# Kernel tuning notes

Hardware: AMD Instinct MI355X
Metric: run time of the kernel (lower is better)

The kernel has to match this reference:

```python
import jax, jax.numpy as jnp
import numpy as np

B, S, C = 32, 1024, 12      # sentences, words per sentence, chars per word
E, H = 256, 512             # embedding dim, word-LSTM hidden dim
V, CS, T = 50000, 128, 50   # vocab, charset, tagset


def _lstm(x, Wih, Whh, b):
    """Standard torch LSTM (gate order i,f,g,o). x: [T, N, I] -> hidden trace [T, N, H]."""
    Hd = Whh.shape[1]
    N = x.shape[1]
    h0 = jnp.zeros((N, Hd), x.dtype)
    c0 = jnp.zeros((N, Hd), x.dtype)

    def step(carry, xt):
        h, c = carry
        gates = xt @ Wih.T + h @ Whh.T + b
        i, f, g, o = jnp.split(gates, 4, axis=-1)
        c = jax.nn.sigmoid(f) * c + jax.nn.sigmoid(i) * jnp.tanh(g)
        h = jax.nn.sigmoid(o) * jnp.tanh(c)
        return (h, c), h

    _, hs = jax.lax.scan(step, (h0, c0), x)
    return hs


def setup_inputs() -> dict:
    key = jax.random.key(0)
    ks = jax.random.split(key, 12)
    sc = 0.05
    return {
        "char_idx": jax.random.randint(ks[0], (B, S, C), 0, CS),
        "word_idx": jax.random.randint(ks[1], (B, S), 0, V),
        "char_emb": jax.random.normal(ks[2], (CS, E), jnp.float32) * sc,
        "word_emb": jax.random.normal(ks[3], (V, E), jnp.float32) * sc,
        "Wc_ih": jax.random.normal(ks[4], (4 * E, E), jnp.float32) * sc,
        "Wc_hh": jax.random.normal(ks[5], (4 * E, E), jnp.float32) * sc,
        "bc": jnp.zeros((4 * E,), jnp.float32),
        "Ww_ih": jax.random.normal(ks[6], (4 * H, 2 * E), jnp.float32) * sc,
        "Ww_hh": jax.random.normal(ks[7], (4 * H, H), jnp.float32) * sc,
        "bw": jnp.zeros((4 * H,), jnp.float32),
        "Wt": jax.random.normal(ks[8], (T, H), jnp.float32) * sc,
        "bt": jnp.zeros((T,), jnp.float32),
    }


def reference(char_idx, word_idx, char_emb, word_emb, Wc_ih, Wc_hh, bc,
              Ww_ih, Ww_hh, bw, Wt, bt):
    # --- character-level LSTM: each word starts from a fresh zero state ---
    ce = char_emb[char_idx]                       # [B, S, C, E]
    ce = ce.reshape(B * S, C, E).transpose(1, 0, 2)  # [C, B*S, E]
    char_hs = _lstm(ce, Wc_ih, Wc_hh, bc)         # [C, B*S, E]
    char_feat = char_hs[-1].reshape(B, S, E)      # last char output per word

    # --- word-level LSTM over concatenated [word_emb ; char_feat] ---
    we = word_emb[word_idx]                       # [B, S, E]
    x = jnp.concatenate([we, char_feat], axis=-1) # [B, S, 2E]
    x = x.transpose(1, 0, 2)                      # [S, B, 2E]
    word_hs = _lstm(x, Ww_ih, Ww_hh, bw)          # [S, B, H]
    word_hs = word_hs.transpose(1, 0, 2)          # [B, S, H]

    # --- tag projection + log_softmax per token ---
    logits = word_hs @ Wt.T + bt                  # [B, S, T]
    return jax.nn.log_softmax(logits, axis=-1)
```

## Files before the change

### kernel.cpp

```cpp
#include <hip/hip_runtime.h>
#include <stdint.h>
#include <stddef.h>

#define NB   32
#define NS   1024
#define NC   12
#define NE   256
#define NH   512
#define NT   50
#define NWRD 32768
#define MC   1024
#define RW   2048
#define KW   512

typedef short bf16x8 __attribute__((ext_vector_type(8)));
typedef short bf16x4 __attribute__((ext_vector_type(4)));
typedef float f32x4  __attribute__((ext_vector_type(4)));
typedef unsigned int u32x4 __attribute__((ext_vector_type(4)));

#define MFMA16(a,b,c) __builtin_amdgcn_mfma_f32_16x16x32_bf16(a, b, c, 0, 0, 0)

__device__ __forceinline__ float bf2f(short u){
  return __uint_as_float(((uint32_t)(uint16_t)u) << 16);
}
__device__ __forceinline__ short f2bf(float f){
  uint32_t u = __float_as_uint(f);
  uint32_t r = (u + 0x7FFFu + ((u >> 16) & 1u)) >> 16;
  return (short)r;
}
__device__ __forceinline__ float sigf(float x){
  float e = __expf(-fabsf(x));
  float s = 1.0f / (1.0f + e);
  return x >= 0.0f ? s : 1.0f - s;
}
__device__ __forceinline__ float tanh_f(float x){
  float e = __expf(-2.0f * fabsf(x));
  float r = (1.0f - e) / (1.0f + e);
  return x >= 0.0f ? r : -r;
}
__device__ __forceinline__ uint32_t agent_ld(const uint32_t* p){
  return __hip_atomic_load(p, __ATOMIC_RELAXED, __HIP_MEMORY_SCOPE_AGENT);
}
__device__ __forceinline__ void agent_st(uint32_t* p, uint32_t v){
  __hip_atomic_store(p, v, __ATOMIC_RELAXED, __HIP_MEMORY_SCOPE_AGENT);
}

__global__ __launch_bounds__(256) void k_prep_pe(
    const float* __restrict__ char_emb, const float* __restrict__ Wc_ih,
    const float* __restrict__ bc, float* __restrict__ PEb)
{
  __shared__ float ce[NE];
  int a = blockIdx.x, tid = threadIdx.x;
  ce[tid] = char_emb[a * NE + tid];
  __syncthreads();
  int j = tid;
  float acc[4];
  #pragma unroll
  for (int g = 0; g < 4; ++g) acc[g] = 0.0f;
  for (int k = 0; k < NE; ++k) {
    float c = ce[k];
    #pragma unroll
    for (int g = 0; g < 4; ++g)
      acc[g] += c * Wc_ih[(size_t)(g * NE + j) * NE + k];
  }
  float4 o;
  o.x = acc[0] + bc[0 * NE + j];
  o.y = acc[1] + bc[1 * NE + j];
  o.z = acc[2] + bc[2 * NE + j];
  o.w = acc[3] + bc[3 * NE + j];
  *(float4*)&PEb[(size_t)a * MC + j * 4] = o;
}

__global__ __launch_bounds__(256) void k_prep_w(
    const float* __restrict__ Wc_hh, const float* __restrict__ Ww_ih,
    const float* __restrict__ Ww_hh, const float* __restrict__ bw,
    short* __restrict__ WhhC, short* __restrict__ WihW,
    short* __restrict__ WhhW, float* __restrict__ bwI)
{
  int r = blockIdx.x;
  int j = r >> 2, g = r & 3, tid = threadIdx.x;
  if (r < MC) {
    float v = Wc_hh[(size_t)(g * NE + j) * NE + tid];
    WhhC[(size_t)r * NE + tid] = f2bf(v);
  }
  #pragma unroll
  for (int kk = 0; kk < 2; ++kk) {
    int k = tid + kk * 256;
    WihW[(size_t)r * KW + k] = f2bf(Ww_ih[(size_t)(g * NH + j) * KW + k]);
    WhhW[(size_t)r * NH + k] = f2bf(Ww_hh[(size_t)(g * NH + j) * NH + k]);
  }
  if (tid == 0) bwI[r] = bw[g * NH + j];
}

__global__ __launch_bounds__(256) void k_char0(
    const int* __restrict__ char_idx, const float* __restrict__ PEb,
    float* __restrict__ c_state, short* __restrict__ h_out)
{
  int w = blockIdx.x, j = threadIdx.x;
  int idx = char_idx[w * NC + 0];
  float4 pe = *(const float4*)&PEb[(size_t)idx * MC + j * 4];
  float c = sigf(pe.x) * tanh_f(pe.z);
  float h = sigf(pe.w) * tanh_f(c);
  c_state[(size_t)w * NE + j] = c;
  h_out[(size_t)w * NE + j] = f2bf(h);
}

template<int KDIM, int EPI>
__global__ __launch_bounds__(256) void gemm_epi(
    const short* __restrict__ Amat, const short* __restrict__ Bmat,
    const float* __restrict__ PEb, const int* __restrict__ char_idx, int tstep,
    float* __restrict__ c_state, short* __restrict__ h_out,
    const float* __restrict__ bias, short* __restrict__ pw_out)
{
  __shared__ __align__(16) short As[128 * 64];
  __shared__ __align__(16) short Bs[128 * 64];
  const int tid = threadIdx.x;
  const int lane = tid & 63;
  const int wid = tid >> 6;
  const int wm = wid >> 1, wn = wid & 1;
  const int m0 = blockIdx.y * 128;
  const int n0 = blockIdx.x * 128;
  const int lo = lane & 15, hi = lane >> 4;

  f32x4 acc[4][4];
  #pragma unroll
  for (int i = 0; i < 4; ++i)
    #pragma unroll
    for (int j = 0; j < 4; ++j) acc[i][j] = (f32x4)0.0f;

  const int nk = KDIM / 64;
  for (int ki = 0; ki < nk; ++ki) {
    __syncthreads();
    #pragma unroll
    for (int it = 0; it < 4; ++it) {
      int cid = tid + it * 256;
      int row = cid >> 3, cp = cid & 7;
      int kch = cp ^ (row & 7);
      *(bf16x8*)&As[row * 64 + cp * 8] =
          *(const bf16x8*)&Amat[(size_t)(m0 + row) * KDIM + ki * 64 + kch * 8];
      *(bf16x8*)&Bs[row * 64 + cp * 8] =
          *(const bf16x8*)&Bmat[(size_t)(n0 + row) * KDIM + ki * 64 + kch * 8];
    }
    __syncthreads();
    #pragma unroll
    for (int kc = 0; kc < 2; ++kc) {
      bf16x8 af[4], bfr[4];
      #pragma unroll
      for (int fm = 0; fm < 4; ++fm) {
        int row = wm * 64 + fm * 16 + lo;
        int ch = (kc * 4 + hi) ^ (row & 7);
        af[fm] = *(bf16x8*)&As[row * 64 + ch * 8];
      }
      #pragma unroll
      for (int fn = 0; fn < 4; ++fn) {
        int row = wn * 64 + fn * 16 + lo;
        int ch = (kc * 4 + hi) ^ (row & 7);
        bfr[fn] = *(bf16x8*)&Bs[row * 64 + ch * 8];
      }
      #pragma unroll
      for (int fm = 0; fm < 4; ++fm)
        #pragma unroll
        for (int fn = 0; fn < 4; ++fn)
          acc[fm][fn] = MFMA16(af[fm], bfr[fn], acc[fm][fn]);
    }
  }

  #pragma unroll
  for (int fm = 0; fm < 4; ++fm) {
    int r0 = m0 + wm * 64 + fm * 16 + hi * 4;
    #pragma unroll
    for (int fn = 0; fn < 4; ++fn) {
      int w = n0 + wn * 64 + fn * 16 + lo;
      if constexpr (EPI == 0) {
        int idx = char_idx[w * NC + tstep];
        float4 pe = *(const float4*)&PEb[(size_t)idx * MC + r0];
        float gi = acc[fm][fn][0] + pe.x;
        float gf = acc[fm][fn][1] + pe.y;
        float gg = acc[fm][fn][2] + pe.z;
        float go = acc[fm][fn][3] + pe.w;
        int j = r0 >> 2;
        float c = sigf(gf) * c_state[(size_t)w * NE + j] + sigf(gi) * tanh_f(gg);
        c_state[(size_t)w * NE + j] = c;
        h_out[(size_t)w * NE + j] = f2bf(sigf(go) * tanh_f(c));
      } else {
        float4 bb = *(const float4*)&bias[r0];
        bf16x4 o;
        o[0] = f2bf(acc[fm][fn][0] + bb.x);
        o[1] = f2bf(acc[fm][fn][1] + bb.y);
        o[2] = f2bf(acc[fm][fn][2] + bb.z);
        o[3] = f2bf(acc[fm][fn][3] + bb.w);
        *(bf16x4*)&pw_out[(size_t)w * RW + r0] = o;
      }
    }
  }
}

__global__ __launch_bounds__(64) void k_xw(
    const int* __restrict__ word_idx, const float* __restrict__ word_emb,
    const short* __restrict__ h_char, short* __restrict__ Xw)
{
  int wp = blockIdx.x;
  int s = wp >> 5, b = wp & 31;
  int w = b * NS + s;
  int tid = threadIdx.x;
  int widx = word_idx[w];
  #pragma unroll
  for (int g = 0; g < 2; ++g) {
    int k4 = (tid + g * 64) * 4;
    bf16x4 o;
    if (k4 < NE) {
      float4 v = *(const float4*)&word_emb[(size_t)widx * NE + k4];
      o[0] = f2bf(v.x); o[1] = f2bf(v.y); o[2] = f2bf(v.z); o[3] = f2bf(v.w);
    } else {
      o = *(const bf16x4*)&h_char[(size_t)w * NE + (k4 - NE)];
    }
    *(bf16x4*)&Xw[(size_t)wp * KW + k4] = o;
  }
}

template<bool FAST>
__device__ __forceinline__ void word_loop(
    const short* __restrict__ Whh, const short* __restrict__ PW,
    short* hdat, uint32_t* flags, short* __restrict__ word_hs,
    short* h_lds, int bk, int tid)
{
  const int lane = tid & 63, wv = tid >> 6;
  const int lo = lane & 15, hi = lane >> 4;
  const int wr = wv >> 1, wc = wv & 1;
  const int rowbase = bk * 64 + wr * 16;
  const int b = wc * 16 + lo;
  const int jl = (rowbase >> 2) + hi;
  const int r4 = rowbase + hi * 4;

  bf16x8 a[16];
  #pragma unroll
  for (int kc = 0; kc < 16; ++kc)
    a[kc] = *(const bf16x8*)&Whh[(size_t)(rowbase + lo) * NH + kc * 32 + hi * 8];

  const int db = tid >> 4, dlo = (tid & 15) * 8;
  const short* dA = hdat + db * 512 + dlo;
  const short* dB = dA + 16384;
  const uint32_t* fA = flags + (lane & 31);
  const uint32_t* fB = fA + 64;

  float cst = 0.0f;
  bf16x4 pw  = *(const bf16x4*)&PW[(size_t)(0 * NB + b) * RW + r4];
  bf16x4 pw1 = *(const bf16x4*)&PW[(size_t)(1 * NB + b) * RW + r4];

  for (int s = 0; s < NS; ++s) {
    const uint32_t tv = (uint32_t)s;
    const int par = s & 1;

    {
      const uint32_t* fp = par ? fB : fA;
      int tries = 0;
      for (;;) {
        uint32_t f;
        if constexpr (FAST)
          asm volatile("global_load_dword %0, %1, off sc0\n\t"
                       "s_waitcnt vmcnt(0)" : "=&v"(f) : "v"(fp));
        else
          asm volatile("global_load_dword %0, %1, off sc1\n\t"
                       "s_waitcnt vmcnt(0)" : "=&v"(f) : "v"(fp));
        if (__ballot(f == tv) == ~0ull) break;
        if constexpr (!FAST) {
          if (++tries > 768) {
            if (__ballot(agent_ld(fp) == tv) == ~0ull) break;
            tries = 0;
          }
        }
        __builtin_amdgcn_s_sleep(1);
      }
    }

    const short* sp = par ? dB : dA;
    bf16x8 d0, d1, d2, d3;
    if constexpr (FAST)
      asm volatile("global_load_dwordx4 %0, %4, off sc0\n\t"
                   "global_load_dwordx4 %1, %4, off offset:256 sc0\n\t"
                   "global_load_dwordx4 %2, %4, off offset:512 sc0\n\t"
                   "global_load_dwordx4 %3, %4, off offset:768 sc0\n\t"
                   "s_waitcnt vmcnt(0)"
                   : "=&v"(d0), "=&v"(d1), "=&v"(d2), "=&v"(d3) : "v"(sp));
    else
      asm volatile("global_load_dwordx4 %0, %4, off sc1\n\t"
                   "global_load_dwordx4 %1, %4, off offset:256 sc1\n\t"
                   "global_load_dwordx4 %2, %4, off offset:512 sc1\n\t"
                   "global_load_dwordx4 %3, %4, off offset:768 sc1\n\t"
                   "s_waitcnt vmcnt(0)"
                   : "=&v"(d0), "=&v"(d1), "=&v"(d2), "=&v"(d3) : "v"(sp));

    int s2 = (s + 2 < NS) ? (s + 2) : (NS - 1);
    bf16x4 pw2 = *(const bf16x4*)&PW[(size_t)(s2 * NB + b) * RW + r4];

    short* buf = h_lds + par * (32 * 520);
    short* dst = buf + db * 520 + dlo;
    *(bf16x8*)&dst[0]   = d0;
    *(bf16x8*)&dst[128] = d1;
    *(bf16x8*)&dst[256] = d2;
    *(bf16x8*)&dst[384] = d3;
    __syncthreads();

    f32x4 acc0, acc1, acc2, acc3;
    #pragma unroll
    for (int q = 0; q < 4; ++q) {
      acc0[q] = bf2f(pw[q]); acc1[q] = 0.0f; acc2[q] = 0.0f; acc3[q] = 0.0f;
    }
    #pragma unroll
    for (int kc = 0; kc < 16; kc += 4) {
      bf16x8 h0 = *(bf16x8*)((const char*)buf + b * 1040 + (kc + 0) * 64 + hi * 16);
      bf16x8 h1 = *(bf16x8*)((const char*)buf + b * 1040 + (kc + 1) * 64 + hi * 16);
      bf16x8 h2 = *(bf16x8*)((const char*)buf + b * 1040 + (kc + 2) * 64 + hi * 16);
      bf16x8 h3 = *(bf16x8*)((const char*)buf + b * 1040 + (kc + 3) * 64 + hi * 16);
      acc0 = MFMA16(a[kc + 0], h0, acc0);
      acc1 = MFMA16(a[kc + 1], h1, acc1);
      acc2 = MFMA16(a[kc + 2], h2, acc2);
      acc3 = MFMA16(a[kc + 3], h3, acc3);
    }
    f32x4 acc;
    #pragma unroll
    for (int q = 0; q < 4; ++q) acc[q] = (acc0[q] + acc1[q]) + (acc2[q] + acc3[q]);

    float c = sigf(acc[1]) * cst + sigf(acc[0]) * tanh_f(acc[2]);
    cst = c;
    short hv = f2bf(sigf(acc[3]) * tanh_f(c));

    unsigned int own = (unsigned int)(unsigned short)hv;
    unsigned int part = (unsigned int)__shfl_xor((int)own, 16);
    const int npar = (s + 1) & 1;
    if ((hi & 1) == 0) {
      unsigned int val = own | (part << 16);
      short* hp = hdat + (npar << 14) + b * 512 + jl;
      if constexpr (FAST)
        asm volatile("global_store_dword %0, %1, off sc0" :: "v"(hp), "v"(val) : "memory");
      else
        asm volatile("global_store_dword %0, %1, off sc1" :: "v"(hp), "v"(val) : "memory");
    }
    asm volatile("s_waitcnt vmcnt(0)" ::: "memory");
    __syncthreads();
    if (tid == 0) {
      uint32_t* fq = flags + npar * 64 + bk;
      if constexpr (FAST)
        asm volatile("global_store_dword %0, %1, off sc0"
                     :: "v"(fq), "v"((uint32_t)(s + 1)) : "memory");
      else
        asm volatile("global_store_dword %0, %1, off sc1"
                     :: "v"(fq), "v"((uint32_t)(s + 1)) : "memory");
    }
    word_hs[((size_t)b * NS + s) * NH + jl] = hv;
    pw = pw1; pw1 = pw2;
  }
}

__global__ __launch_bounds__(512, 2) void k_word(
    const short* __restrict__ Whh,
    const short* __restrict__ PW,
    uint8_t* __restrict__ xb,
    short* __restrict__ word_hs)
{
  __shared__ __align__(16) short h_lds[2 * 32 * 520];
  __shared__ int sh_bk, sh_fast;
  const int tid = threadIdx.x;

  short*    hdat  = (short*)xb;
  uint32_t* flags = (uint32_t*)(xb + 65536);
  uint32_t* cnt   = (uint32_t*)(xb + 66048);
  uint32_t* win   = (uint32_t*)(xb + 66080);
  uint32_t* probe = (uint32_t*)(xb + 66112);
  uint32_t* rdy1  = (uint32_t*)(xb + 66240);
  uint32_t* ack1  = (uint32_t*)(xb + 66368);
  uint32_t* rdy2  = (uint32_t*)(xb + 66496);
  uint32_t* verd  = (uint32_t*)(xb + 66624);

  if (tid == 0) {
    uint32_t xcc;
    asm volatile("s_getreg_b32 %0, hwreg(HW_REG_XCC_ID)" : "=s"(xcc));
    xcc &= 7u;
    uint32_t slot = __hip_atomic_fetch_add(&cnt[xcc], 1u, __ATOMIC_RELAXED,
                                           __HIP_MEMORY_SCOPE_AGENT);
    if (slot == 31u) {
      uint32_t exp = 0u;
      __hip_atomic_compare_exchange_strong(win, &exp, xcc + 1u, __ATOMIC_RELAXED,
                                           __ATOMIC_RELAXED, __HIP_MEMORY_SCOPE_AGENT);
    }
    uint32_t w;
    for (;;) {
      w = agent_ld(win);
      if (w != 0u) break;
      __builtin_amdgcn_s_sleep(8);
    }
    sh_bk = (w == xcc + 1u && slot < 32u) ? (int)slot : -1;
  }
  __syncthreads();
  const int bk = sh_bk;
  if (bk < 0) return;

  if (tid == 0) {
    if (bk == 0) {
      asm volatile("global_store_dword %0, %1, off sc0" :: "v"(probe), "v"(0x11111111u) : "memory");
      asm volatile("s_waitcnt vmcnt(0)" ::: "memory");
      agent_st(rdy1, 1u);
      uint32_t a;
      for (;;) { a = agent_ld(ack1); if (a != 0u) break; __builtin_amdgcn_s_sleep(4); }
      if (a == 1u) {
        asm volatile("global_store_dword %0, %1, off sc0" :: "v"(probe), "v"(0x22222222u) : "memory");
        asm volatile("s_waitcnt vmcnt(0)" ::: "memory");
        agent_st(rdy2, 1u);
      }
    } else if (bk == 31) {
      for (;;) { if (agent_ld(rdy1) != 0u) break; __builtin_amdgcn_s_sleep(4); }
      bool okA = false;
      for (int i = 0; i < 192 && !okA; ++i) {
        uint32_t pv;
        asm volatile("global_load_dword %0, %1, off sc0\n\ts_waitcnt vmcnt(0)"
                     : "=&v"(pv) : "v"(probe));
        okA = (pv == 0x11111111u);
        if (!okA) __builtin_amdgcn_s_sleep(2);
      }
      agent_st(ack1, okA ? 1u : 2u);
      bool okB = false;
      if (okA) {
        for (;;) { if (agent_ld(rdy2) != 0u) break; __builtin_amdgcn_s_sleep(4); }
        for (int i = 0; i < 192 && !okB; ++i) {
          uint32_t pv;
          asm volatile("global_load_dword %0, %1, off sc0\n\ts_waitcnt vmcnt(0)"
                       : "=&v"(pv) : "v"(probe));
          okB = (pv == 0x22222222u);
          if (!okB) __builtin_amdgcn_s_sleep(2);
        }
      }
      agent_st(verd, okB ? 1u : 2u);
    }
    uint32_t v;
    for (;;) { v = agent_ld(verd); if (v != 0u) break; __builtin_amdgcn_s_sleep(4); }
    sh_fast = (v == 1u);
  }
  __syncthreads();

  if (sh_fast)
    word_loop<true >(Whh, PW, hdat, flags, word_hs, h_lds, bk, tid);
  else
    word_loop<false>(Whh, PW, hdat, flags, word_hs, h_lds, bk, tid);
}

__global__ __launch_bounds__(256) void k_tags(
    const short* __restrict__ word_hs, const float* __restrict__ Wt,
    const float* __restrict__ bt, float* __restrict__ out)
{
  __shared__ __align__(16) short Ws[64 * 256];
  const int tid = threadIdx.x, lane = tid & 63, wid = tid >> 6;
  const int lo = lane & 15, hi = lane >> 4;
  const int n0 = blockIdx.x * 128;
  const int wb = n0 + wid * 32;

  f32x4 acc[4][2];
  #pragma unroll
  for (int fm = 0; fm < 4; ++fm)
    #pragma unroll
    for (int fn = 0; fn < 2; ++fn) acc[fm][fn] = (f32x4)0.0f;

  for (int half = 0; half < 2; ++half) {
    __syncthreads();
    for (int cid = tid; cid < 2048; cid += 256) {
      int row = cid >> 5, cp = cid & 31;
      int kch = cp ^ (row & 7);
      bf16x8 v;
      if (row < NT) {
        const float* src = &Wt[(size_t)row * KW + half * 256 + kch * 8];
        #pragma unroll
        for (int e = 0; e < 8; ++e) v[e] = f2bf(src[e]);
      } else v = (bf16x8)0;
      *(bf16x8*)&Ws[row * 256 + cp * 8] = v;
    }
    __syncthreads();
    #pragma unroll
    for (int kc = 0; kc < 8; ++kc) {
      bf16x8 bfr[2];
      #pragma unroll
      for (int fn = 0; fn < 2; ++fn) {
        int w = wb + fn * 16 + lo;
        bfr[fn] = *(const bf16x8*)&word_hs[(size_t)w * KW + half * 256 + kc * 32 + hi * 8];
      }
      #pragma unroll
      for (int fm = 0; fm < 4; ++fm) {
        int row = fm * 16 + lo;
        int ch = (kc * 4 + hi) ^ (row & 7);
        bf16x8 av = *(bf16x8*)&Ws[row * 256 + ch * 8];
        acc[fm][0] = MFMA16(av, bfr[0], acc[fm][0]);
        acc[fm][1] = MFMA16(av, bfr[1], acc[fm][1]);
      }
    }
  }

  #pragma unroll
  for (int fn = 0; fn < 2; ++fn) {
    int w = wb + fn * 16 + lo;
    float lg[16];
    float m = -1e30f;
    #pragma unroll
    for (int fm = 0; fm < 4; ++fm)
      #pragma unroll
      for (int q = 0; q < 4; ++q) {
        int tg = fm * 16 + hi * 4 + q;
        float bv = (tg < NT) ? bt[tg] : 0.0f;
        float v = acc[fm][fn][q] + bv;
        lg[fm * 4 + q] = v;
        if (tg < NT) m = fmaxf(m, v);
      }
    m = fmaxf(m, __shfl_xor(m, 16));
    m = fmaxf(m, __shfl_xor(m, 32));
    float s = 0.0f;
    #pragma unroll
    for (int fm = 0; fm < 4; ++fm)
      #pragma unroll
      for (int q = 0; q < 4; ++q) {
        int tg = fm * 16 + hi * 4 + q;
        if (tg < NT) s += __expf(lg[fm * 4 + q] - m);
      }
    s += __shfl_xor(s, 16);
    s += __shfl_xor(s, 32);
    float lz = m + __logf(s);
    #pragma unroll
    for (int fm = 0; fm < 4; ++fm)
      #pragma unroll
      for (int q = 0; q < 4; ++q) {
        int tg = fm * 16 + hi * 4 + q;
        if (tg < NT) out[(size_t)w * NT + tg] = lg[fm * 4 + q] - lz;
      }
  }
}

extern "C" void kernel_launch(void* const* d_in, const int* in_sizes, int n_in,
                              void* d_out, int out_size, void* d_ws, size_t ws_size,
                              hipStream_t stream) {
  const int*   char_idx = (const int*)  d_in[0];
  const int*   word_idx = (const int*)  d_in[1];
  const float* char_emb = (const float*)d_in[2];
  const float* word_emb = (const float*)d_in[3];
  const float* Wc_ih    = (const float*)d_in[4];
  const float* Wc_hh    = (const float*)d_in[5];
  const float* bc       = (const float*)d_in[6];
  const float* Ww_ih    = (const float*)d_in[7];
  const float* Ww_hh    = (const float*)d_in[8];
  const float* bw       = (const float*)d_in[9];
  const float* Wt       = (const float*)d_in[10];
  const float* bt       = (const float*)d_in[11];
  float* out = (float*)d_out;

  const size_t MB = 1ull << 20;
  uint8_t* w8 = (uint8_t*)d_ws;
  float* PEb   = (float*)(w8 + 0);
  short* WhhC  = (short*)(w8 + 512 * 1024);
  short* WihW  = (short*)(w8 + 1 * MB);
  short* WhhW  = (short*)(w8 + 3 * MB);
  float* bwI   = (float*)(w8 + 5 * MB);
  uint8_t* xb  = (uint8_t*)(w8 + 5 * MB + 64 * 1024);
  short* hA    = (short*)(w8 + 6 * MB);
  short* hB    = (short*)(w8 + 22 * MB);
  short* whs   = (short*)(w8 + 6 * MB);
  float* cC    = (float*)(w8 + 38 * MB);
  short* Xw    = (short*)(w8 + 38 * MB);
  short* PW    = (short*)(w8 + 70 * MB);

  k_prep_pe<<<128, 256, 0, stream>>>(char_emb, Wc_ih, bc, PEb);
  k_prep_w<<<2048, 256, 0, stream>>>(Wc_hh, Ww_ih, Ww_hh, bw, WhhC, WihW, WhhW, bwI);

  k_char0<<<NWRD, 256, 0, stream>>>(char_idx, PEb, cC, hA);
  for (int t = 1; t < NC; ++t) {
    short* src = (t & 1) ? hA : hB;
    short* dst = (t & 1) ? hB : hA;
    gemm_epi<256, 0><<<dim3(256, 8), 256, 0, stream>>>(
        WhhC, src, PEb, char_idx, t, cC, dst, nullptr, nullptr);
  }

  k_xw<<<NWRD, 64, 0, stream>>>(word_idx, word_emb, hB, Xw);
  gemm_epi<512, 1><<<dim3(256, 16), 256, 0, stream>>>(
      WihW, Xw, nullptr, nullptr, 0, nullptr, nullptr, bwI, PW);

  hipMemsetAsync(xb, 0, 67584, stream);
  k_word<<<256, 512, 0, stream>>>(WhhW, PW, xb, whs);

  k_tags<<<256, 256, 0, stream>>>(whs, Wt, bt, out);
}
```

Baseline: 3.976 ms.

## Halve word-LSTM block threads, each wave computes two 16-row gate tiles

The persistent word-LSTM kernel now runs 256 threads (4 waves) per block instead of 512. Each wave keeps two 16-row slices of the recurrent weight matrix in registers and issues twice as many MFMAs per step against the same shared-memory h tile. Each thread also loads 8 vectors of the broadcast hidden state instead of 4. The aim is fewer waves taking part in the per-step __syncthreads and flag polling, and fewer redundant LDS h reads. In exchange the register pressure per thread doubles (32 bf16x8 weight fragments), which could cause spills, and per-wave serial work per step grows.

```diff
diff --git a/kernel.cpp b/kernel.cpp
--- a/kernel.cpp
+++ b/kernel.cpp
@@ -227,25 +227,30 @@
   const int lane = tid & 63, wv = tid >> 6;
   const int lo = lane & 15, hi = lane >> 4;
   const int wr = wv >> 1, wc = wv & 1;
-  const int rowbase = bk * 64 + wr * 16;
+  const int rowbase = bk * 64 + wr * 32;
   const int b = wc * 16 + lo;
-  const int jl = (rowbase >> 2) + hi;
-  const int r4 = rowbase + hi * 4;
-
-  bf16x8 a[16];
-  #pragma unroll
-  for (int kc = 0; kc < 16; ++kc)
-    a[kc] = *(const bf16x8*)&Whh[(size_t)(rowbase + lo) * NH + kc * 32 + hi * 8];
-
-  const int db = tid >> 4, dlo = (tid & 15) * 8;
+  const int jbase = (rowbase >> 2) + hi;
+  const int r4a = rowbase + hi * 4;
+  const int r4b = rowbase + 16 + hi * 4;
+
+  bf16x8 a0[16], a1[16];
+  #pragma unroll
+  for (int kc = 0; kc < 16; ++kc) {
+    a0[kc] = *(const bf16x8*)&Whh[(size_t)(rowbase + lo) * NH + kc * 32 + hi * 8];
+    a1[kc] = *(const bf16x8*)&Whh[(size_t)(rowbase + 16 + lo) * NH + kc * 32 + hi * 8];
+  }
+
+  const int db = tid >> 3, dlo = (tid & 7) * 8;
   const short* dA = hdat + db * 512 + dlo;
   const short* dB = dA + 16384;
   const uint32_t* fA = flags + (lane & 31);
   const uint32_t* fB = fA + 64;
 
-  float cst = 0.0f;
-  bf16x4 pw  = *(const bf16x4*)&PW[(size_t)(0 * NB + b) * RW + r4];
-  bf16x4 pw1 = *(const bf16x4*)&PW[(size_t)(1 * NB + b) * RW + r4];
+  float cst0 = 0.0f, cst1 = 0.0f;
+  bf16x4 pwa  = *(const bf16x4*)&PW[(size_t)(0 * NB + b) * RW + r4a];
+  bf16x4 pwb  = *(const bf16x4*)&PW[(size_t)(0 * NB + b) * RW + r4b];
+  bf16x4 pwa1 = *(const bf16x4*)&PW[(size_t)(1 * NB + b) * RW + r4a];
+  bf16x4 pwb1 = *(const bf16x4*)&PW[(size_t)(1 * NB + b) * RW + r4b];
 
   for (int s = 0; s < NS; ++s) {
     const uint32_t tv = (uint32_t)s;
@@ -274,67 +279,104 @@
     }
 
     const short* sp = par ? dB : dA;
-    bf16x8 d0, d1, d2, d3;
-    if constexpr (FAST)
+    bf16x8 d0, d1, d2, d3, d4, d5, d6, d7;
+    if constexpr (FAST) {
       asm volatile("global_load_dwordx4 %0, %4, off sc0\n\t"
-                   "global_load_dwordx4 %1, %4, off offset:256 sc0\n\t"
-                   "global_load_dwordx4 %2, %4, off offset:512 sc0\n\t"
-                   "global_load_dwordx4 %3, %4, off offset:768 sc0\n\t"
+                   "global_load_dwordx4 %1, %4, off offset:128 sc0\n\t"
+                   "global_load_dwordx4 %2, %4, off offset:256 sc0\n\t"
+                   "global_load_dwordx4 %3, %4, off offset:384 sc0"
+                   : "=&v"(d0), "=&v"(d1), "=&v"(d2), "=&v"(d3) : "v"(sp));
+      asm volatile("global_load_dwordx4 %0, %4, off offset:512 sc0\n\t"
+                   "global_load_dwordx4 %1, %4, off offset:640 sc0\n\t"
+                   "global_load_dwordx4 %2, %4, off offset:768 sc0\n\t"
+                   "global_load_dwordx4 %3, %4, off offset:896 sc0\n\t"
                    "s_waitcnt vmcnt(0)"
+                   : "=&v"(d4), "=&v"(d5), "=&v"(d6), "=&v"(d7) : "v"(sp));
+    } else {
+      asm volatile("global_load_dwordx4 %0, %4, off sc1\n\t"
+                   "global_load_dwordx4 %1, %4, off offset:128 sc1\n\t"
+                   "global_load_dwordx4 %2, %4, off offset:256 sc1\n\t"
+                   "global_load_dwordx4 %3, %4, off offset:384 sc1"
                    : "=&v"(d0), "=&v"(d1), "=&v"(d2), "=&v"(d3) : "v"(sp));
-    else
-      asm volatile("global_load_dwordx4 %0, %4, off sc1\n\t"
-                   "global_load_dwordx4 %1, %4, off offset:256 sc1\n\t"
-                   "global_load_dwordx4 %2, %4, off offset:512 sc1\n\t"
-                   "global_load_dwordx4 %3, %4, off offset:768 sc1\n\t"
+      asm volatile("global_load_dwordx4 %0, %4, off offset:512 sc1\n\t"
+                   "global_load_dwordx4 %1, %4, off offset:640 sc1\n\t"
+                   "global_load_dwordx4 %2, %4, off offset:768 sc1\n\t"
+                   "global_load_dwordx4 %3, %4, off offset:896 sc1\n\t"
                    "s_waitcnt vmcnt(0)"
-                   : "=&v"(d0), "=&v"(d1), "=&v"(d2), "=&v"(d3) : "v"(sp));
+                   : "=&v"(d4), "=&v"(d5), "=&v"(d6), "=&v"(d7) : "v"(sp));
+    }
 
     int s2 = (s + 2 < NS) ? (s + 2) : (NS - 1);
-    bf16x4 pw2 = *(const bf16x4*)&PW[(size_t)(s2 * NB + b) * RW + r4];
+    bf16x4 pwa2 = *(const bf16x4*)&PW[(size_t)(s2 * NB + b) * RW + r4a];
+    bf16x4 pwb2 = *(const bf16x4*)&PW[(size_t)(s2 * NB + b) * RW + r4b];
 
     short* buf = h_lds + par * (32 * 520);
     short* dst = buf + db * 520 + dlo;
     *(bf16x8*)&dst[0]   = d0;
-    *(bf16x8*)&dst[128] = d1;
-    *(bf16x8*)&dst[256] = d2;
-    *(bf16x8*)&dst[384] = d3;
+    *(bf16x8*)&dst[64]  = d1;
+    *(bf16x8*)&dst[128] = d2;
+    *(bf16x8*)&dst[192] = d3;
+    *(bf16x8*)&dst[256] = d4;
+    *(bf16x8*)&dst[320] = d5;
+    *(bf16x8*)&dst[384] = d6;
+    *(bf16x8*)&dst[448] = d7;
     __syncthreads();
 
-    f32x4 acc0, acc1, acc2, acc3;
+    f32x4 ac0[4], ac1[4];
     #pragma unroll
     for (int q = 0; q < 4; ++q) {
-      acc0[q] = bf2f(pw[q]); acc1[q] = 0.0f; acc2[q] = 0.0f; acc3[q] = 0.0f;
-    }
+      ac0[0][q] = bf2f(pwa[q]); ac1[0][q] = bf2f(pwb[q]);
+    }
+    #pragma unroll
+    for (int c = 1; c < 4; ++c)
+      #pragma unroll
+      for (int q = 0; q < 4; ++q) { ac0[c][q] = 0.0f; ac1[c][q] = 0.0f; }
     #pragma unroll
     for (int kc = 0; kc < 16; kc += 4) {
       bf16x8 h0 = *(bf16x8*)((const char*)buf + b * 1040 + (kc + 0) * 64 + hi * 16);
       bf16x8 h1 = *(bf16x8*)((const char*)buf + b * 1040 + (kc + 1) * 64 + hi * 16);
       bf16x8 h2 = *(bf16x8*)((const char*)buf + b * 1040 + (kc + 2) * 64 + hi * 16);
       bf16x8 h3 = *(bf16x8*)((const char*)buf + b * 1040 + (kc + 3) * 64 + hi * 16);
-      acc0 = MFMA16(a[kc + 0], h0, acc0);
-      acc1 = MFMA16(a[kc + 1], h1, acc1);
-      acc2 = MFMA16(a[kc + 2], h2, acc2);
-      acc3 = MFMA16(a[kc + 3], h3, acc3);
-    }
-    f32x4 acc;
-    #pragma unroll
-    for (int q = 0; q < 4; ++q) acc[q] = (acc0[q] + acc1[q]) + (acc2[q] + acc3[q]);
-
-    float c = sigf(acc[1]) * cst + sigf(acc[0]) * tanh_f(acc[2]);
-    cst = c;
-    short hv = f2bf(sigf(acc[3]) * tanh_f(c));
-
-    unsigned int own = (unsigned int)(unsigned short)hv;
-    unsigned int part = (unsigned int)__shfl_xor((int)own, 16);
+      ac0[0] = MFMA16(a0[kc + 0], h0, ac0[0]);
+      ac1[0] = MFMA16(a1[kc + 0], h0, ac1[0]);
+      ac0[1] = MFMA16(a0[kc + 1], h1, ac0[1]);
+      ac1[1] = MFMA16(a1[kc + 1], h1, ac1[1]);
+      ac0[2] = MFMA16(a0[kc + 2], h2, ac0[2]);
+      ac1[2] = MFMA16(a1[kc + 2], h2, ac1[2]);
+      ac0[3] = MFMA16(a0[kc + 3], h3, ac0[3]);
+      ac1[3] = MFMA16(a1[kc + 3], h3, ac1[3]);
+    }
+    f32x4 accA, accB;
+    #pragma unroll
+    for (int q = 0; q < 4; ++q) {
+      accA[q] = (ac0[0][q] + ac0[1][q]) + (ac0[2][q] + ac0[3][q]);
+      accB[q] = (ac1[0][q] + ac1[1][q]) + (ac1[2][q] + ac1[3][q]);
+    }
+
+    float c0 = sigf(accA[1]) * cst0 + sigf(accA[0]) * tanh_f(accA[2]);
+    cst0 = c0;
+    short hv0 = f2bf(sigf(accA[3]) * tanh_f(c0));
+    float c1 = sigf(accB[1]) * cst1 + sigf(accB[0]) * tanh_f(accB[2]);
+    cst1 = c1;
+    short hv1 = f2bf(sigf(accB[3]) * tanh_f(c1));
+
+    unsigned int own0 = (unsigned int)(unsigned short)hv0;
+    unsigned int own1 = (unsigned int)(unsigned short)hv1;
+    unsigned int part0 = (unsigned int)__shfl_xor((int)own0, 16);
+    unsigned int part1 = (unsigned int)__shfl_xor((int)own1, 16);
     const int npar = (s + 1) & 1;
     if ((hi & 1) == 0) {
-      unsigned int val = own | (part << 16);
-      short* hp = hdat + (npar << 14) + b * 512 + jl;
-      if constexpr (FAST)
-        asm volatile("global_store_dword %0, %1, off sc0" :: "v"(hp), "v"(val) : "memory");
-      else
-        asm volatile("global_store_dword %0, %1, off sc1" :: "v"(hp), "v"(val) : "memory");
+      unsigned int v0 = own0 | (part0 << 16);
+      unsigned int v1 = own1 | (part1 << 16);
+      short* hp0 = hdat + (npar << 14) + b * 512 + jbase;
+      short* hp1 = hp0 + 4;
+      if constexpr (FAST) {
+        asm volatile("global_store_dword %0, %1, off sc0" :: "v"(hp0), "v"(v0) : "memory");
+        asm volatile("global_store_dword %0, %1, off sc0" :: "v"(hp1), "v"(v1) : "memory");
+      } else {
+        asm volatile("global_store_dword %0, %1, off sc1" :: "v"(hp0), "v"(v0) : "memory");
+        asm volatile("global_store_dword %0, %1, off sc1" :: "v"(hp1), "v"(v1) : "memory");
+      }
     }
     asm volatile("s_waitcnt vmcnt(0)" ::: "memory");
     __syncthreads();
@@ -347,12 +389,14 @@
         asm volatile("global_store_dword %0, %1, off sc1"
                      :: "v"(fq), "v"((uint32_t)(s + 1)) : "memory");
     }
-    word_hs[((size_t)b * NS + s) * NH + jl] = hv;
-    pw = pw1; pw1 = pw2;
-  }
-}
-
-__global__ __launch_bounds__(512, 2) void k_word(
+    word_hs[((size_t)b * NS + s) * NH + jbase]     = hv0;
+    word_hs[((size_t)b * NS + s) * NH + jbase + 4] = hv1;
+    pwa = pwa1; pwa1 = pwa2;
+    pwb = pwb1; pwb1 = pwb2;
+  }
+}
+
+__global__ __launch_bounds__(256, 1) void k_word(
     const short* __restrict__ Whh,
     const short* __restrict__ PW,
     uint8_t* __restrict__ xb,
@@ -578,7 +622,7 @@
       WihW, Xw, nullptr, nullptr, 0, nullptr, nullptr, bwI, PW);
 
   hipMemsetAsync(xb, 0, 67584, stream);
-  k_word<<<256, 512, 0, stream>>>(WhhW, PW, xb, whs);
+  k_word<<<256, 256, 0, stream>>>(WhhW, PW, xb, whs);
 
   k_tags<<<256, 256, 0, stream>>>(whs, Wt, bt, out);
 }
```

New measurement: 4.532 ms. 14.0% more time.
